# Optimization experiments

Measured on AMD Instinct MI355X. Metric: run time of the kernel, lower is better.

## Reference

```python
import jax, jax.numpy as jnp
import numpy as np

EPS = 1e-6
NUM_HEADS = 4
GSIZE = (2, 2, 2)


def _ln_channels_first(x, w, b):
    # LayerNorm over channel dim (axis=1) of [B,C,D,H,W]
    u = x.mean(1, keepdims=True)
    s = ((x - u) ** 2).mean(1, keepdims=True)
    xn = (x - u) / jnp.sqrt(s + EPS)
    return w[None, :, None, None, None] * xn + b[None, :, None, None, None]


def setup_inputs() -> dict:
    key = jax.random.key(0)
    ks = jax.random.split(key, 7)
    B, C = 2, 256
    x2 = jax.random.normal(ks[0], (B, C, 32, 32, 32), jnp.float32)
    x1_low = jax.random.normal(ks[1], (B, C, 16, 16, 16), jnp.float32)
    sc = 1.0 / np.sqrt(C).astype(np.float32)
    q_w = jax.random.normal(ks[2], (C, C), jnp.float32) * sc
    k_w = jax.random.normal(ks[3], (C, C), jnp.float32) * sc
    v_w = jax.random.normal(ks[4], (C, C), jnp.float32) * sc
    dw_w = jax.random.normal(ks[5], (C, 1, 3, 3, 3), jnp.float32) * (1.0 / np.sqrt(27.0).astype(np.float32))
    proj_w = jax.random.normal(ks[6], (C, C), jnp.float32) * sc
    nq_w = jnp.ones((C,), jnp.float32)
    nq_b = jnp.zeros((C,), jnp.float32)
    nkv_w = jnp.ones((C,), jnp.float32)
    nkv_b = jnp.zeros((C,), jnp.float32)
    return {"x2": x2, "x1_low": x1_low, "q_w": q_w, "k_w": k_w, "v_w": v_w,
            "dw_w": dw_w, "proj_w": proj_w, "nq_w": nq_w, "nq_b": nq_b,
            "nkv_w": nkv_w, "nkv_b": nkv_b}


def reference(x2, x1_low, q_w, k_w, v_w, dw_w, proj_w, nq_w, nq_b, nkv_w, nkv_b):
    B, C, D, H, W = x2.shape
    h = NUM_HEADS
    d = C // h
    gD, gH, gW = GSIZE
    _, _, Dl, Hl, Wl = x1_low.shape

    # adaptive_avg_pool3d to (gD,gH,gW): dims divisible -> block means
    tokens = x1_low.reshape(B, C, gD, Dl // gD, gH, Hl // gH, gW, Wl // gW).mean((3, 5, 7))
    # depthwise 3x3x3 conv, padding 1
    dw = jax.lax.conv_general_dilated(
        tokens, dw_w, window_strides=(1, 1, 1), padding='SAME',
        dimension_numbers=('NCDHW', 'OIDHW', 'NCDHW'), feature_group_count=C)
    tokens = tokens + dw

    N = D * H * W
    g = gD * gH * gW

    qx = _ln_channels_first(x2, nq_w, nq_b).reshape(B, C, N)
    q = jnp.einsum('oc,bcn->bon', q_w, qx).reshape(B, h, d, N).transpose(0, 1, 3, 2)  # [B,h,N,d]

    tk = _ln_channels_first(tokens, nkv_w, nkv_b).reshape(B, C, g)
    k = jnp.einsum('oc,bcg->bog', k_w, tk).reshape(B, h, d, g)  # [B,h,d,g]
    v = jnp.einsum('oc,bcg->bog', v_w, tokens.reshape(B, C, g)).reshape(B, h, d, g).transpose(0, 1, 3, 2)  # [B,h,g,d]

    attn = jax.nn.softmax(jnp.einsum('bhnd,bhdg->bhng', q, k) / jnp.sqrt(jnp.float32(d)), axis=-1)
    out = jnp.einsum('bhng,bhgd->bhnd', attn, v)  # [B,h,N,d]
    out = out.transpose(0, 1, 3, 2).reshape(B, C, N)
    return jnp.einsum('oc,bcn->bon', proj_w, out).reshape(B, C, D, H, W)
```

## Files before the change

kernel.cpp:

```cpp
#include <hip/hip_runtime.h>
#include <math.h>

#define EPS 1e-6f

typedef __attribute__((ext_vector_type(8))) short bhalf8;
typedef __attribute__((ext_vector_type(4))) float floatx4;

__device__ __forceinline__ unsigned short f2bf(float f) {
    union { float f; unsigned u; } v; v.f = f;
    unsigned r = (v.u + 0x7fffu + ((v.u >> 16) & 1u)) >> 16;
    return (unsigned short)r;
}
__device__ __forceinline__ float bflo(unsigned u) {
    union { unsigned x; float f; } v; v.x = u << 16; return v.f;
}
__device__ __forceinline__ float bfhi(unsigned u) {
    union { unsigned x; float f; } v; v.x = u & 0xffff0000u; return v.f;
}

__global__ void pre1(const float* __restrict__ q_w,
                     const float* __restrict__ proj_w,
                     const float* __restrict__ nq_w,
                     const float* __restrict__ nq_b,
                     unsigned short* __restrict__ W1b,
                     unsigned short* __restrict__ W2b,
                     float* __restrict__ A, float* __restrict__ Bc,
                     const float* __restrict__ x1, float* __restrict__ tokens) {
    if (blockIdx.x < 256) {
        int o = blockIdx.x;
        int c = threadIdx.x;
        float qv = q_w[o * 256 + c];
        float pv = proj_w[o * 256 + c];
        float w1 = qv * nq_w[c];
        int kc = c >> 5, kk = c & 31;
        W1b[kc * 8192 + o * 32 + kk] = f2bf(w1);
        W2b[kc * 8192 + o * 32 + kk] = f2bf(pv);
        float bcv = qv * nq_b[c];
        __shared__ float sA[4], sB[4];
        float a = w1, b = bcv;
        for (int off = 32; off > 0; off >>= 1) {
            a += __shfl_down(a, off);
            b += __shfl_down(b, off);
        }
        int wave = threadIdx.x >> 6, lane = threadIdx.x & 63;
        if (lane == 0) { sA[wave] = a; sB[wave] = b; }
        __syncthreads();
        if (threadIdx.x == 0) {
            A[o]  = sA[0] + sA[1] + sA[2] + sA[3];
            Bc[o] = sB[0] + sB[1] + sB[2] + sB[3];
        }
    } else {
        int bc = blockIdx.x - 256;
        const float* base = x1 + (size_t)bc * 4096;
        int wave = threadIdx.x >> 6;
        int lane = threadIdx.x & 63;
        int doff = lane >> 3, hoff = lane & 7;
        for (int t = wave * 2; t < wave * 2 + 2; ++t) {
            int gd = t >> 2, gh = (t >> 1) & 1, gw = t & 1;
            const float* p = base + (gd * 8 + doff) * 256 + (gh * 8 + hoff) * 16 + gw * 8;
            float4 v0 = *(const float4*)p;
            float4 v1 = *(const float4*)(p + 4);
            float s = v0.x + v0.y + v0.z + v0.w + v1.x + v1.y + v1.z + v1.w;
            for (int off = 32; off > 0; off >>= 1) s += __shfl_down(s, off);
            if (lane == 0) tokens[bc * 8 + t] = s * (1.0f / 512.0f);
        }
    }
}

__global__ void tokens_all(const float* __restrict__ tokens,
                           const float* __restrict__ dw_w,
                           const float* __restrict__ nkv_w,
                           const float* __restrict__ nkv_b,
                           const float* __restrict__ k_w,
                           const float* __restrict__ v_w,
                           unsigned short* __restrict__ kkb,
                           float* __restrict__ vv) {
    int b = blockIdx.x >> 6;
    int og = blockIdx.x & 63;
    int c = threadIdx.x;
    __shared__ float t2[256][9];
    __shared__ float u8[8], r8[8];
    float t[8];
    #pragma unroll
    for (int g = 0; g < 8; ++g) t[g] = tokens[(b * 256 + c) * 8 + g];
    float w[27];
    #pragma unroll
    for (int i = 0; i < 27; ++i) w[i] = dw_w[c * 27 + i];
    #pragma unroll
    for (int z = 0; z < 2; ++z)
    #pragma unroll
    for (int y = 0; y < 2; ++y)
    #pragma unroll
    for (int x = 0; x < 2; ++x) {
        float s = 0.f;
        #pragma unroll
        for (int i = 0; i < 3; ++i) {
            int nz = z + i - 1; if (nz < 0 || nz > 1) continue;
            #pragma unroll
            for (int j = 0; j < 3; ++j) {
                int ny = y + j - 1; if (ny < 0 || ny > 1) continue;
                #pragma unroll
                for (int l = 0; l < 3; ++l) {
                    int nx = x + l - 1; if (nx < 0 || nx > 1) continue;
                    s += w[(i * 3 + j) * 3 + l] * t[nz * 4 + ny * 2 + nx];
                }
            }
        }
        int g = z * 4 + y * 2 + x;
        t2[c][g] = t[g] + s;
    }
    __syncthreads();
    if (c < 8) {
        float su = 0.f, sq = 0.f;
        for (int cc = 0; cc < 256; ++cc) { float v = t2[cc][c]; su += v; sq += v * v; }
        float u = su * (1.f / 256.f);
        float var = sq * (1.f / 256.f) - u * u;
        u8[c] = u;
        r8[c] = rsqrtf(var + EPS);
    }
    __syncthreads();
    int wv = threadIdx.x >> 6;
    int lane = threadIdx.x & 63;
    int o = og * 4 + wv;
    float acck[8] = {0,0,0,0,0,0,0,0}, accv[8] = {0,0,0,0,0,0,0,0};
    #pragma unroll
    for (int i = 0; i < 4; ++i) {
        int cc = lane + 64 * i;
        float kw = k_w[o * 256 + cc];
        float vw = v_w[o * 256 + cc];
        float nw = nkv_w[cc], nb2 = nkv_b[cc];
        #pragma unroll
        for (int g = 0; g < 8; ++g) {
            float tv = t2[cc][g];
            acck[g] += kw * (nw * (tv - u8[g]) * r8[g] + nb2);
            accv[g] += vw * tv;
        }
    }
    #pragma unroll
    for (int g = 0; g < 8; ++g)
        for (int off = 32; off > 0; off >>= 1) {
            acck[g] += __shfl_down(acck[g], off);
            accv[g] += __shfl_down(accv[g], off);
        }
    if (lane == 0) {
        #pragma unroll
        for (int g = 0; g < 8; ++g) {
            kkb[b * 2048 + o * 8 + g] = f2bf(acck[g]);
            vv[b * 2048 + (o >> 6) * 512 + g * 64 + (o & 63)] = accv[g];
        }
    }
}

__global__ __launch_bounds__(256, 5)
void fused2(const float* __restrict__ x2,
            const unsigned short* __restrict__ W1b,
            const unsigned short* __restrict__ W2b,
            const float* __restrict__ Ag, const float* __restrict__ Bg,
            const unsigned short* __restrict__ kkb,
            const float* __restrict__ vvf,
            float* __restrict__ out) {
    __shared__ __align__(16) unsigned short XQ[8192];
    __shared__ __align__(16) float KVP[3072];
    __shared__ __align__(16) float part[256];
    __shared__ __align__(16) float As[256], Bs[256];
    __shared__ float us[32], rs[32];

    const int tid = threadIdx.x;
    const int w = tid >> 6;
    const int lane = tid & 63;
    const int n0g = blockIdx.x * 32;
    const int b = n0g >> 15;
    const int pos0 = n0g & 32767;

    uint4  kreg  = ((const uint4*)(kkb + b * 2048))[tid];
    float4 vreg0 = ((const float4*)(vvf + b * 2048))[tid];
    float4 vreg1 = ((const float4*)(vvf + b * 2048))[256 + tid];
    As[tid] = Ag[tid];
    Bs[tid] = Bg[tid];

    {
        const int n4 = tid & 7, cg = tid >> 3;
        const float* xb = x2 + (size_t)b * 8388608 + pos0 + n4 * 4;
        float su[4] = {0,0,0,0}, sq[4] = {0,0,0,0};
        #pragma unroll
        for (int cc = 0; cc < 4; ++cc) {
            int p = cg + 32 * cc;
            int c0 = 2 * p;
            float4 a  = *(const float4*)(xb + (size_t)c0 * 32768);
            float4 bq = *(const float4*)(xb + (size_t)(c0 + 1) * 32768);
            int g = p >> 2, wsub = p & 3;
            float av[4] = {a.x, a.y, a.z, a.w};
            float bv[4] = {bq.x, bq.y, bq.z, bq.w};
            #pragma unroll
            for (int i = 0; i < 4; ++i) {
                su[i] += av[i] + bv[i];
                sq[i] += av[i] * av[i] + bv[i] * bv[i];
                int row = 4 * n4 + i;
                int swz = ((row >> 2) ^ row) & 7;
                unsigned val = (unsigned)f2bf(av[i]) | ((unsigned)f2bf(bv[i]) << 16);
                ((unsigned*)XQ)[row * 128 + ((g ^ swz) << 2) + wsub] = val;
            }
        }
        ((uint4*)KVP)[tid] = kreg;
        float* vs0 = KVP + 1024;
        ((float4*)vs0)[tid]       = vreg0;
        ((float4*)vs0)[256 + tid] = vreg1;
        #pragma unroll
        for (int i = 0; i < 4; ++i) {
            float a2 = su[i], q2 = sq[i];
            a2 += __shfl_down(a2, 8);  q2 += __shfl_down(q2, 8);
            a2 += __shfl_down(a2, 16); q2 += __shfl_down(q2, 16);
            a2 += __shfl_down(a2, 32); q2 += __shfl_down(q2, 32);
            if (lane < 8) {
                part[w * 64 + lane * 8 + i * 2]     = a2;
                part[w * 64 + lane * 8 + i * 2 + 1] = q2;
            }
        }
    }
    __syncthreads();

    if (tid < 32) {
        int n4 = tid >> 2, i = tid & 3;
        float S = 0.f, Q = 0.f;
        #pragma unroll
        for (int w4 = 0; w4 < 4; ++w4) {
            S += part[w4 * 64 + n4 * 8 + i * 2];
            Q += part[w4 * 64 + n4 * 8 + i * 2 + 1];
        }
        float mu = S * (1.f / 256.f);
        us[tid] = mu;
        rs[tid] = rsqrtf(Q * (1.f / 256.f) - mu * mu + EPS);
    }

    const int m = lane & 15;
    const int qd = lane >> 4;

    floatx4 acc[4][2];
    #pragma unroll
    for (int i = 0; i < 4; ++i) {
        acc[i][0] = (floatx4){0.f, 0.f, 0.f, 0.f};
        acc[i][1] = (floatx4){0.f, 0.f, 0.f, 0.f};
    }
    const unsigned short* w1p = W1b + (size_t)(64 * w + m) * 32 + qd * 8;
    {
        bhalf8 afb[2][4];
        #pragma unroll
        for (int t = 0; t < 4; ++t) afb[0][t] = *(const bhalf8*)(w1p + t * 512);
        #pragma unroll
        for (int kc = 0; kc < 8; ++kc) {
            if (kc < 7) {
                #pragma unroll
                for (int t = 0; t < 4; ++t)
                    afb[(kc + 1) & 1][t] = *(const bhalf8*)(w1p + (kc + 1) * 8192 + t * 512);
            }
            bhalf8 bfr[2];
            #pragma unroll
            for (int nt = 0; nt < 2; ++nt) {
                int n = nt * 16 + m;
                int swz = ((n >> 2) ^ n) & 7;
                bfr[nt] = *(const bhalf8*)(XQ + n * 256 + (((4 * kc + qd) ^ swz) << 3));
            }
            #pragma unroll
            for (int t = 0; t < 4; ++t)
                #pragma unroll
                for (int nt = 0; nt < 2; ++nt)
                    acc[t][nt] = __builtin_amdgcn_mfma_f32_16x16x32_bf16(afb[kc & 1][t], bfr[nt], acc[t][nt], 0, 0, 0);
        }
    }
    __syncthreads();

    #pragma unroll
    for (int t = 0; t < 4; ++t) {
        int ob = 64 * w + 16 * t + 4 * qd;
        floatx4 Af = *(const floatx4*)&As[ob];
        floatx4 Bf = *(const floatx4*)&Bs[ob];
        int gq = ob >> 3, off = ob & 7;
        #pragma unroll
        for (int nt = 0; nt < 2; ++nt) {
            int n = nt * 16 + m;
            int swz = ((n >> 2) ^ n) & 7;
            float uv = us[n], rv = rs[n];
            unsigned p0 = (unsigned)f2bf(rv * (acc[t][nt][0] - uv * Af[0]) + Bf[0])
                        | ((unsigned)f2bf(rv * (acc[t][nt][1] - uv * Af[1]) + Bf[1]) << 16);
            unsigned p1 = (unsigned)f2bf(rv * (acc[t][nt][2] - uv * Af[2]) + Bf[2])
                        | ((unsigned)f2bf(rv * (acc[t][nt][3] - uv * Af[3]) + Bf[3]) << 16);
            uint2 val; val.x = p0; val.y = p1;
            *(uint2*)(XQ + n * 256 + ((gq ^ swz) << 3) + off) = val;
        }
    }

    {
        const int an = lane & 31, dh = lane >> 5;
        const int sw = ((an >> 2) ^ an) & 7;
        unsigned short* qrow = XQ + an * 256;
        uint4 q4[4];
        #pragma unroll
        for (int gl = 0; gl < 4; ++gl)
            q4[gl] = *(const uint4*)(qrow + (((8 * w + 4 * dh + gl) ^ sw) << 3));
        float lg[8] = {0, 0, 0, 0, 0, 0, 0, 0};
        const unsigned short* kh = (const unsigned short*)KVP + w * 512 + dh * 256;
        #pragma unroll
        for (int dp = 0; dp < 16; ++dp) {
            unsigned qq = ((const unsigned*)q4)[dp];
            float q0 = bflo(qq), q1 = bfhi(qq);
            uint4 k0 = *(const uint4*)(kh + dp * 16);
            uint4 k1 = *(const uint4*)(kh + dp * 16 + 8);
            lg[0] += q0 * bflo(k0.x); lg[1] += q0 * bfhi(k0.x);
            lg[2] += q0 * bflo(k0.y); lg[3] += q0 * bfhi(k0.y);
            lg[4] += q0 * bflo(k0.z); lg[5] += q0 * bfhi(k0.z);
            lg[6] += q0 * bflo(k0.w); lg[7] += q0 * bfhi(k0.w);
            lg[0] += q1 * bflo(k1.x); lg[1] += q1 * bfhi(k1.x);
            lg[2] += q1 * bflo(k1.y); lg[3] += q1 * bfhi(k1.y);
            lg[4] += q1 * bflo(k1.z); lg[5] += q1 * bfhi(k1.z);
            lg[6] += q1 * bflo(k1.w); lg[7] += q1 * bfhi(k1.w);
        }
        #pragma unroll
        for (int g = 0; g < 8; ++g) lg[g] += __shfl_xor(lg[g], 32);
        float mx = lg[0];
        #pragma unroll
        for (int g = 1; g < 8; ++g) mx = fmaxf(mx, lg[g]);
        float p[8], s = 0.f;
        #pragma unroll
        for (int g = 0; g < 8; ++g) { p[g] = __expf((lg[g] - mx) * 0.125f); s += p[g]; }
        float is = 1.f / s;
        #pragma unroll
        for (int g = 0; g < 8; ++g) p[g] *= is;
        float o2[32];
        #pragma unroll
        for (int j = 0; j < 32; ++j) o2[j] = 0.f;
        const float* vh = KVP + 1024 + w * 512 + dh * 32;
        #pragma unroll
        for (int g = 0; g < 8; ++g) {
            float pg = p[g];
            #pragma unroll
            for (int j = 0; j < 8; ++j) {
                float4 v4 = *(const float4*)(vh + g * 64 + j * 4);
                o2[4 * j + 0] += pg * v4.x;
                o2[4 * j + 1] += pg * v4.y;
                o2[4 * j + 2] += pg * v4.z;
                o2[4 * j + 3] += pg * v4.w;
            }
        }
        #pragma unroll
        for (int gl = 0; gl < 4; ++gl) {
            uint4 pk;
            pk.x = (unsigned)f2bf(o2[8 * gl + 0]) | ((unsigned)f2bf(o2[8 * gl + 1]) << 16);
            pk.y = (unsigned)f2bf(o2[8 * gl + 2]) | ((unsigned)f2bf(o2[8 * gl + 3]) << 16);
            pk.z = (unsigned)f2bf(o2[8 * gl + 4]) | ((unsigned)f2bf(o2[8 * gl + 5]) << 16);
            pk.w = (unsigned)f2bf(o2[8 * gl + 6]) | ((unsigned)f2bf(o2[8 * gl + 7]) << 16);
            *(uint4*)(qrow + (((8 * w + 4 * dh + gl) ^ sw) << 3)) = pk;
        }
    }
    __syncthreads();

    floatx4 acc2[4][2];
    #pragma unroll
    for (int i = 0; i < 4; ++i) {
        acc2[i][0] = (floatx4){0.f, 0.f, 0.f, 0.f};
        acc2[i][1] = (floatx4){0.f, 0.f, 0.f, 0.f};
    }
    const unsigned short* w2p = W2b + (size_t)(64 * w + m) * 32 + qd * 8;
    {
        bhalf8 afb[2][4];
        #pragma unroll
        for (int t = 0; t < 4; ++t) afb[0][t] = *(const bhalf8*)(w2p + t * 512);
        #pragma unroll
        for (int kc = 0; kc < 8; ++kc) {
            if (kc < 7) {
                #pragma unroll
                for (int t = 0; t < 4; ++t)
                    afb[(kc + 1) & 1][t] = *(const bhalf8*)(w2p + (kc + 1) * 8192 + t * 512);
            }
            bhalf8 bfr[2];
            #pragma unroll
            for (int nt = 0; nt < 2; ++nt) {
                int n = nt * 16 + m;
                int swz = ((n >> 2) ^ n) & 7;
                bfr[nt] = *(const bhalf8*)(XQ + n * 256 + (((4 * kc + qd) ^ swz) << 3));
            }
            #pragma unroll
            for (int t = 0; t < 4; ++t)
                #pragma unroll
                for (int nt = 0; nt < 2; ++nt)
                    acc2[t][nt] = __builtin_amdgcn_mfma_f32_16x16x32_bf16(afb[kc & 1][t], bfr[nt], acc2[t][nt], 0, 0, 0);
        }
    }

    {
        float* tb = KVP + w * 320;
        float* obase = out + (size_t)b * 8388608 + pos0;
        const int ol = lane >> 2, c4 = lane & 3;
        #pragma unroll
        for (int t = 0; t < 4; ++t) {
            #pragma unroll
            for (int nt = 0; nt < 2; ++nt) {
                #pragma unroll
                for (int rr = 0; rr < 4; ++rr)
                    tb[(qd * 4 + rr) * 20 + m] = acc2[t][nt][rr];
                float4 vo = *(const float4*)(tb + ol * 20 + c4 * 4);
                *(float4*)(obase + (size_t)(64 * w + 16 * t + ol) * 32768 + nt * 16 + c4 * 4) = vo;
            }
        }
    }
}

extern "C" void kernel_launch(void* const* d_in, const int* in_sizes, int n_in,
                              void* d_out, int out_size, void* d_ws, size_t ws_size,
                              hipStream_t stream) {
    (void)in_sizes; (void)n_in; (void)out_size; (void)ws_size;
    const float* x2     = (const float*)d_in[0];
    const float* x1_low = (const float*)d_in[1];
    const float* q_w    = (const float*)d_in[2];
    const float* k_w    = (const float*)d_in[3];
    const float* v_w    = (const float*)d_in[4];
    const float* dw_w   = (const float*)d_in[5];
    const float* proj_w = (const float*)d_in[6];
    const float* nq_w   = (const float*)d_in[7];
    const float* nq_b   = (const float*)d_in[8];
    const float* nkv_w  = (const float*)d_in[9];
    const float* nkv_b  = (const float*)d_in[10];
    float* outp = (float*)d_out;

    float* wsf = (float*)d_ws;
    float* Av  = wsf;
    float* Bv  = wsf + 256;
    float* tk  = wsf + 512;
    float* vvf = wsf + 4608;
    unsigned short* kkb = (unsigned short*)(wsf + 8704);
    unsigned short* W1b = (unsigned short*)(wsf + 10752);
    unsigned short* W2b = (unsigned short*)(wsf + 43520);

    pre1<<<768, 256, 0, stream>>>(q_w, proj_w, nq_w, nq_b, W1b, W2b, Av, Bv, x1_low, tk);
    tokens_all<<<128, 256, 0, stream>>>(tk, dw_w, nkv_w, nkv_b, k_w, v_w, kkb, vvf);
    fused2<<<2048, 256, 0, stream>>>(x2, W1b, W2b, Av, Bv, kkb, vvf, outp);
}
```

Baseline: 187.8 us.

## Double fused kernel tile to 64 positions with 512-thread blocks

The fused attention kernel now handles 64 spatial positions per block using 8 waves instead of 32 positions with 4 waves. Each wave computes 32 output channels across 64 positions, so every weight fragment loaded from global memory feeds twice as many MFMAs and total weight traffic per position halves. It also preloads the first weight fragments for both GEMMs earlier so their latency overlaps with the x2 load and the LayerNorm reduction. In exchange it needs more shared memory per block, adds a barrier before the attention stage, and launches half as many blocks, which may reduce occupancy.

```diff
diff --git a/kernel.cpp b/kernel.cpp
--- a/kernel.cpp
+++ b/kernel.cpp
@@ -151,7 +151,7 @@
     }
 }
 
-__global__ __launch_bounds__(256, 5)
+__global__ __launch_bounds__(512, 6)
 void fused2(const float* __restrict__ x2,
             const unsigned short* __restrict__ W1b,
             const unsigned short* __restrict__ W2b,
@@ -159,27 +159,31 @@
             const unsigned short* __restrict__ kkb,
             const float* __restrict__ vvf,
             float* __restrict__ out) {
-    __shared__ __align__(16) unsigned short XQ[8192];
+    __shared__ __align__(16) unsigned short XQ[16384];
     __shared__ __align__(16) float KVP[3072];
-    __shared__ __align__(16) float part[256];
+    __shared__ __align__(16) float part[1024];
     __shared__ __align__(16) float As[256], Bs[256];
-    __shared__ float us[32], rs[32];
+    __shared__ float us[64], rs[64];
 
     const int tid = threadIdx.x;
     const int w = tid >> 6;
     const int lane = tid & 63;
-    const int n0g = blockIdx.x * 32;
+    const int m = lane & 15;
+    const int qd = lane >> 4;
+    const int n0g = blockIdx.x * 64;
     const int b = n0g >> 15;
     const int pos0 = n0g & 32767;
 
-    uint4  kreg  = ((const uint4*)(kkb + b * 2048))[tid];
-    float4 vreg0 = ((const float4*)(vvf + b * 2048))[tid];
-    float4 vreg1 = ((const float4*)(vvf + b * 2048))[256 + tid];
-    As[tid] = Ag[tid];
-    Bs[tid] = Bg[tid];
+    uint4 kreg;
+    if (tid < 256) kreg = ((const uint4*)(kkb + b * 2048))[tid];
+    float4 vreg = ((const float4*)(vvf + b * 2048))[tid];
+    if (tid < 256) { As[tid] = Ag[tid]; Bs[tid] = Bg[tid]; }
+    const unsigned short* w1p = W1b + (size_t)(32 * w + m) * 32 + qd * 8;
+    bhalf8 af1_0 = *(const bhalf8*)(w1p);
+    bhalf8 af1_1 = *(const bhalf8*)(w1p + 512);
 
     {
-        const int n4 = tid & 7, cg = tid >> 3;
+        const int n4 = tid & 15, cg = tid >> 4;
         const float* xb = x2 + (size_t)b * 8388608 + pos0 + n4 * 4;
         float su[4] = {0,0,0,0}, sq[4] = {0,0,0,0};
         #pragma unroll
@@ -201,82 +205,75 @@
                 ((unsigned*)XQ)[row * 128 + ((g ^ swz) << 2) + wsub] = val;
             }
         }
-        ((uint4*)KVP)[tid] = kreg;
-        float* vs0 = KVP + 1024;
-        ((float4*)vs0)[tid]       = vreg0;
-        ((float4*)vs0)[256 + tid] = vreg1;
+        if (tid < 256) ((uint4*)KVP)[tid] = kreg;
+        ((float4*)(KVP + 1024))[tid] = vreg;
         #pragma unroll
         for (int i = 0; i < 4; ++i) {
             float a2 = su[i], q2 = sq[i];
-            a2 += __shfl_down(a2, 8);  q2 += __shfl_down(q2, 8);
             a2 += __shfl_down(a2, 16); q2 += __shfl_down(q2, 16);
             a2 += __shfl_down(a2, 32); q2 += __shfl_down(q2, 32);
-            if (lane < 8) {
-                part[w * 64 + lane * 8 + i * 2]     = a2;
-                part[w * 64 + lane * 8 + i * 2 + 1] = q2;
-            }
-        }
-    }
-    __syncthreads();
-
-    if (tid < 32) {
-        int n4 = tid >> 2, i = tid & 3;
+            if (lane < 16) {
+                part[w * 128 + (4 * lane + i) * 2]     = a2;
+                part[w * 128 + (4 * lane + i) * 2 + 1] = q2;
+            }
+        }
+    }
+    __syncthreads();
+
+    if (tid < 64) {
         float S = 0.f, Q = 0.f;
         #pragma unroll
-        for (int w4 = 0; w4 < 4; ++w4) {
-            S += part[w4 * 64 + n4 * 8 + i * 2];
-            Q += part[w4 * 64 + n4 * 8 + i * 2 + 1];
+        for (int w8 = 0; w8 < 8; ++w8) {
+            S += part[w8 * 128 + tid * 2];
+            Q += part[w8 * 128 + tid * 2 + 1];
         }
         float mu = S * (1.f / 256.f);
         us[tid] = mu;
         rs[tid] = rsqrtf(Q * (1.f / 256.f) - mu * mu + EPS);
     }
 
-    const int m = lane & 15;
-    const int qd = lane >> 4;
-
-    floatx4 acc[4][2];
-    #pragma unroll
-    for (int i = 0; i < 4; ++i) {
-        acc[i][0] = (floatx4){0.f, 0.f, 0.f, 0.f};
-        acc[i][1] = (floatx4){0.f, 0.f, 0.f, 0.f};
-    }
-    const unsigned short* w1p = W1b + (size_t)(64 * w + m) * 32 + qd * 8;
+    floatx4 acc[2][4];
+    #pragma unroll
+    for (int i = 0; i < 2; ++i)
+        #pragma unroll
+        for (int j = 0; j < 4; ++j)
+            acc[i][j] = (floatx4){0.f, 0.f, 0.f, 0.f};
     {
-        bhalf8 afb[2][4];
-        #pragma unroll
-        for (int t = 0; t < 4; ++t) afb[0][t] = *(const bhalf8*)(w1p + t * 512);
+        bhalf8 afb[2][2];
+        afb[0][0] = af1_0; afb[0][1] = af1_1;
         #pragma unroll
         for (int kc = 0; kc < 8; ++kc) {
             if (kc < 7) {
-                #pragma unroll
-                for (int t = 0; t < 4; ++t)
-                    afb[(kc + 1) & 1][t] = *(const bhalf8*)(w1p + (kc + 1) * 8192 + t * 512);
-            }
-            bhalf8 bfr[2];
-            #pragma unroll
-            for (int nt = 0; nt < 2; ++nt) {
+                afb[(kc + 1) & 1][0] = *(const bhalf8*)(w1p + (kc + 1) * 8192);
+                afb[(kc + 1) & 1][1] = *(const bhalf8*)(w1p + (kc + 1) * 8192 + 512);
+            }
+            bhalf8 bfr[4];
+            #pragma unroll
+            for (int nt = 0; nt < 4; ++nt) {
                 int n = nt * 16 + m;
                 int swz = ((n >> 2) ^ n) & 7;
                 bfr[nt] = *(const bhalf8*)(XQ + n * 256 + (((4 * kc + qd) ^ swz) << 3));
             }
             #pragma unroll
-            for (int t = 0; t < 4; ++t)
+            for (int t = 0; t < 2; ++t)
                 #pragma unroll
-                for (int nt = 0; nt < 2; ++nt)
+                for (int nt = 0; nt < 4; ++nt)
                     acc[t][nt] = __builtin_amdgcn_mfma_f32_16x16x32_bf16(afb[kc & 1][t], bfr[nt], acc[t][nt], 0, 0, 0);
         }
     }
-    __syncthreads();
-
-    #pragma unroll
-    for (int t = 0; t < 4; ++t) {
-        int ob = 64 * w + 16 * t + 4 * qd;
+    const unsigned short* w2p = W2b + (size_t)(32 * w + m) * 32 + qd * 8;
+    bhalf8 af2_0 = *(const bhalf8*)(w2p);
+    bhalf8 af2_1 = *(const bhalf8*)(w2p + 512);
+    __syncthreads();
+
+    #pragma unroll
+    for (int t = 0; t < 2; ++t) {
+        int ob = 32 * w + 16 * t + 4 * qd;
         floatx4 Af = *(const floatx4*)&As[ob];
         floatx4 Bf = *(const floatx4*)&Bs[ob];
         int gq = ob >> 3, off = ob & 7;
         #pragma unroll
-        for (int nt = 0; nt < 2; ++nt) {
+        for (int nt = 0; nt < 4; ++nt) {
             int n = nt * 16 + m;
             int swz = ((n >> 2) ^ n) & 7;
             float uv = us[n], rv = rs[n];
@@ -288,17 +285,20 @@
             *(uint2*)(XQ + n * 256 + ((gq ^ swz) << 3) + off) = val;
         }
     }
+    __syncthreads();
 
     {
-        const int an = lane & 31, dh = lane >> 5;
+        const int h = w & 3;
+        const int an = ((w >> 2) << 5) | (lane & 31);
+        const int dh = lane >> 5;
         const int sw = ((an >> 2) ^ an) & 7;
         unsigned short* qrow = XQ + an * 256;
         uint4 q4[4];
         #pragma unroll
         for (int gl = 0; gl < 4; ++gl)
-            q4[gl] = *(const uint4*)(qrow + (((8 * w + 4 * dh + gl) ^ sw) << 3));
+            q4[gl] = *(const uint4*)(qrow + (((8 * h + 4 * dh + gl) ^ sw) << 3));
         float lg[8] = {0, 0, 0, 0, 0, 0, 0, 0};
-        const unsigned short* kh = (const unsigned short*)KVP + w * 512 + dh * 256;
+        const unsigned short* kh = (const unsigned short*)KVP + h * 512 + dh * 256;
         #pragma unroll
         for (int dp = 0; dp < 16; ++dp) {
             unsigned qq = ((const unsigned*)q4)[dp];
@@ -328,7 +328,7 @@
         float o2[32];
         #pragma unroll
         for (int j = 0; j < 32; ++j) o2[j] = 0.f;
-        const float* vh = KVP + 1024 + w * 512 + dh * 32;
+        const float* vh = KVP + 1024 + h * 512 + dh * 32;
         #pragma unroll
         for (int g = 0; g < 8; ++g) {
             float pg = p[g];
@@ -348,40 +348,37 @@
             pk.y = (unsigned)f2bf(o2[8 * gl + 2]) | ((unsigned)f2bf(o2[8 * gl + 3]) << 16);
             pk.z = (unsigned)f2bf(o2[8 * gl + 4]) | ((unsigned)f2bf(o2[8 * gl + 5]) << 16);
             pk.w = (unsigned)f2bf(o2[8 * gl + 6]) | ((unsigned)f2bf(o2[8 * gl + 7]) << 16);
-            *(uint4*)(qrow + (((8 * w + 4 * dh + gl) ^ sw) << 3)) = pk;
-        }
-    }
-    __syncthreads();
-
-    floatx4 acc2[4][2];
-    #pragma unroll
-    for (int i = 0; i < 4; ++i) {
-        acc2[i][0] = (floatx4){0.f, 0.f, 0.f, 0.f};
-        acc2[i][1] = (floatx4){0.f, 0.f, 0.f, 0.f};
-    }
-    const unsigned short* w2p = W2b + (size_t)(64 * w + m) * 32 + qd * 8;
+            *(uint4*)(qrow + (((8 * h + 4 * dh + gl) ^ sw) << 3)) = pk;
+        }
+    }
+    __syncthreads();
+
+    floatx4 acc2[2][4];
+    #pragma unroll
+    for (int i = 0; i < 2; ++i)
+        #pragma unroll
+        for (int j = 0; j < 4; ++j)
+            acc2[i][j] = (floatx4){0.f, 0.f, 0.f, 0.f};
     {
-        bhalf8 afb[2][4];
-        #pragma unroll
-        for (int t = 0; t < 4; ++t) afb[0][t] = *(const bhalf8*)(w2p + t * 512);
+        bhalf8 afb[2][2];
+        afb[0][0] = af2_0; afb[0][1] = af2_1;
         #pragma unroll
         for (int kc = 0; kc < 8; ++kc) {
             if (kc < 7) {
-                #pragma unroll
-                for (int t = 0; t < 4; ++t)
-                    afb[(kc + 1) & 1][t] = *(const bhalf8*)(w2p + (kc + 1) * 8192 + t * 512);
-            }
-            bhalf8 bfr[2];
-            #pragma unroll
-            for (int nt = 0; nt < 2; ++nt) {
+                afb[(kc + 1) & 1][0] = *(const bhalf8*)(w2p + (kc + 1) * 8192);
+                afb[(kc + 1) & 1][1] = *(const bhalf8*)(w2p + (kc + 1) * 8192 + 512);
+            }
+            bhalf8 bfr[4];
+            #pragma unroll
+            for (int nt = 0; nt < 4; ++nt) {
                 int n = nt * 16 + m;
                 int swz = ((n >> 2) ^ n) & 7;
                 bfr[nt] = *(const bhalf8*)(XQ + n * 256 + (((4 * kc + qd) ^ swz) << 3));
             }
             #pragma unroll
-            for (int t = 0; t < 4; ++t)
+            for (int t = 0; t < 2; ++t)
                 #pragma unroll
-                for (int nt = 0; nt < 2; ++nt)
+                for (int nt = 0; nt < 4; ++nt)
                     acc2[t][nt] = __builtin_amdgcn_mfma_f32_16x16x32_bf16(afb[kc & 1][t], bfr[nt], acc2[t][nt], 0, 0, 0);
         }
     }
@@ -391,14 +388,14 @@
         float* obase = out + (size_t)b * 8388608 + pos0;
         const int ol = lane >> 2, c4 = lane & 3;
         #pragma unroll
-        for (int t = 0; t < 4; ++t) {
-            #pragma unroll
-            for (int nt = 0; nt < 2; ++nt) {
+        for (int t = 0; t < 2; ++t) {
+            #pragma unroll
+            for (int nt = 0; nt < 4; ++nt) {
                 #pragma unroll
                 for (int rr = 0; rr < 4; ++rr)
                     tb[(qd * 4 + rr) * 20 + m] = acc2[t][nt][rr];
                 float4 vo = *(const float4*)(tb + ol * 20 + c4 * 4);
-                *(float4*)(obase + (size_t)(64 * w + 16 * t + ol) * 32768 + nt * 16 + c4 * 4) = vo;
+                *(float4*)(obase + (size_t)(32 * w + 16 * t + ol) * 32768 + nt * 16 + c4 * 4) = vo;
             }
         }
     }
@@ -432,5 +429,5 @@
 
     pre1<<<768, 256, 0, stream>>>(q_w, proj_w, nq_w, nq_b, W1b, W2b, Av, Bv, x1_low, tk);
     tokens_all<<<128, 256, 0, stream>>>(tk, dw_w, nkv_w, nkv_b, k_w, v_w, kkb, vvf);
-    fused2<<<2048, 256, 0, stream>>>(x2, W1b, W2b, Av, Bv, kkb, vvf, outp);
-}
+    fused2<<<1024, 512, 0, stream>>>(x2, W1b, W2b, Av, Bv, kkb, vvf, outp);
+}
```

Result: slower. 253.0 us (+34.7%).
